# Kernel tuning notes

Measured on AMD Instinct MI355X. Metric: run time of the kernel, lower is better.

## Reference

```python
import jax, jax.numpy as jnp
import numpy as np

B, N, DIN, DH, DOUT, H = 2, 512, 32, 64, 64, 4
NEG_SLOPE = 0.2  # PyG GATv2Conv default
EPS = 1e-5       # LayerNorm eps


def layernorm(y, g, b):
    mu = jnp.mean(y, axis=-1, keepdims=True)
    var = jnp.mean(jnp.square(y - mu), axis=-1, keepdims=True)
    return (y - mu) * jax.lax.rsqrt(var + EPS) * g + b


def gatv2(x, wl, bl, wr, br, att, bias, mask):
    """Dense GATv2 over all-pairs edges given boolean mask [N,N] (j->i)."""
    Bb, Nn, _ = x.shape
    Hh, Dd = att.shape
    xl = (x @ wl + bl).reshape(Bb, Nn, Hh, Dd)  # source features W_l x_j
    xr = (x @ wr + br).reshape(Bb, Nn, Hh, Dd)  # target features W_r x_i
    # e[b,h,i,j] = att_h . leaky_relu(xl[b,j,h] + xr[b,i,h])
    z = jax.nn.leaky_relu(xl[:, None, :, :, :] + xr[:, :, None, :, :], NEG_SLOPE)  # [B,i,j,H,D]
    e = jnp.einsum('bijhd,hd->bhij', z, att)
    e = jnp.where(mask[None, None], e, -jnp.inf)
    alpha = jax.nn.softmax(e, axis=-1)            # softmax over source j per target i
    out = jnp.einsum('bhij,bjhd->bihd', alpha, xl).reshape(Bb, Nn, Hh * Dd)
    return out + bias


def setup_inputs() -> dict:
    key = jax.random.key(0)
    ks = jax.random.split(key, 10)
    s = lambda k, shape: (jax.random.normal(k, shape, dtype=jnp.float32) * 0.1)
    return {
        'x': jax.random.normal(ks[0], (B, N, DIN), dtype=jnp.float32),
        'embedding': jax.random.normal(ks[1], (N, DH), dtype=jnp.float32),
        # gat1: in_dim -> hidden_dim, 4 heads, concat
        'w1_l': s(ks[2], (DIN, H * DH)), 'b1_l': jnp.zeros((H * DH,), jnp.float32),
        'w1_r': s(ks[3], (DIN, H * DH)), 'b1_r': jnp.zeros((H * DH,), jnp.float32),
        'att1': s(ks[4], (H, DH)), 'bias1': jnp.zeros((H * DH,), jnp.float32),
        'g1': jnp.ones((H * DH,), jnp.float32), 'be1': jnp.zeros((H * DH,), jnp.float32),
        # gat2: 4*hidden_dim -> out_dim, 4 heads, concat
        'w2_l': s(ks[5], (H * DH, H * DOUT)), 'b2_l': jnp.zeros((H * DOUT,), jnp.float32),
        'w2_r': s(ks[6], (H * DH, H * DOUT)), 'b2_r': jnp.zeros((H * DOUT,), jnp.float32),
        'att2': s(ks[7], (H, DOUT)), 'bias2': jnp.zeros((H * DOUT,), jnp.float32),
        'g2': jnp.ones((H * DOUT,), jnp.float32), 'be2': jnp.zeros((H * DOUT,), jnp.float32),
    }


def reference(x, embedding, w1_l, b1_l, w1_r, b1_r, att1, bias1, g1, be1,
              w2_l, b2_l, w2_r, b2_r, att2, bias2, g2, be2):
    # AdaptiveAdjacency: cosine-similarity adjacency; only its nonzero
    # PATTERN is used (edge_index = adj.nonzero()); self-loops added by GATv2Conv.
    ne = embedding * jax.lax.rsqrt(jnp.sum(embedding * embedding, axis=1, keepdims=True))
    adj = ne @ ne.T
    mask = (adj != 0) | jnp.eye(N, dtype=bool)
    h = gatv2(x, w1_l, b1_l, w1_r, b1_r, att1, bias1, mask)
    h = jax.nn.relu(layernorm(h, g1, be1))
    # dropout(p=0.3) is identity in eval mode
    out = gatv2(h, w2_l, b2_l, w2_r, b2_r, att2, bias2, mask)
    out = layernorm(out, g2, be2)
    return out
```

## Files before the change

kernel.cpp:

```cpp
#include <hip/hip_runtime.h>


#define BB   2
#define NN   512
#define DIN  32
#define DH   64
#define HH   4
#define C1   256
#define C2   256
#define NJC  4
#define LEPS 1e-5f

typedef unsigned long long u64;

__device__ __forceinline__ float bf_sum(float v) {
#pragma unroll
    for (int o = 32; o > 0; o >>= 1) v += __shfl_xor(v, o, 64);
    return v;
}

__device__ __forceinline__ void gload_lds16(const float* g, float* l) {
    __builtin_amdgcn_global_load_lds(
        (const __attribute__((address_space(1))) void*)g,
        (__attribute__((address_space(3))) void*)l, 16, 0, 0);
}

__device__ __forceinline__ float rdlane(float v, int l) {
    return __int_as_float(__builtin_amdgcn_readlane(__float_as_int(v), l));
}

__global__ __launch_bounds__(256) void mask_k(const float* __restrict__ emb,
                                              u64* __restrict__ mask64) {
    __shared__ __align__(16) float s_ei[16][DH];
    __shared__ float ebuf[64][DH + 1];
    int it = blockIdx.x, jq = blockIdx.y;
    int t = threadIdx.x, lane = t & 63, iq = t >> 6;
    int j0 = jq * 64;
    {
        int row = t >> 4, d4 = (t & 15) << 2;
        *(float4*)&s_ei[row][d4] = *(const float4*)(emb + (it * 16 + row) * DH + d4);
    }
#pragma unroll
    for (int k = 0; k < 4; k++) {
        int idx = k * 256 + t, jl = idx >> 4, d4 = (idx & 15) << 2;
        float4 v = *(const float4*)(emb + (j0 + jl) * DH + d4);
        ebuf[jl][d4] = v.x; ebuf[jl][d4 + 1] = v.y;
        ebuf[jl][d4 + 2] = v.z; ebuf[jl][d4 + 3] = v.w;
    }
    __syncthreads();
    float acc[4] = {0.f, 0.f, 0.f, 0.f};
    for (int dc = 0; dc < 16; dc++) {
        int d = dc * 4;
        float e0 = ebuf[lane][d], e1 = ebuf[lane][d + 1];
        float e2 = ebuf[lane][d + 2], e3 = ebuf[lane][d + 3];
#pragma unroll
        for (int r = 0; r < 4; r++) {
            float4 iv = *(const float4*)&s_ei[iq * 4 + r][d];
            acc[r] += iv.x * e0 + iv.y * e1 + iv.z * e2 + iv.w * e3;
        }
    }
    int jg = j0 + lane;
#pragma unroll
    for (int r = 0; r < 4; r++) {
        int ig = it * 16 + iq * 4 + r;
        u64 bal = __ballot(acc[r] != 0.f || ig == jg);
        if (lane == 0) mask64[ig * 8 + jq] = bal;
    }
}

__global__ __launch_bounds__(256) void proj1_k(const float* __restrict__ x,
        const float* __restrict__ wl, const float* __restrict__ bl,
        const float* __restrict__ wr, const float* __restrict__ br,
        const float* __restrict__ att,
        float* __restrict__ xl, float* __restrict__ xr,
        float* __restrict__ sl, float* __restrict__ sr) {
    __shared__ float s_x[4][DIN];
    int t = threadIdx.x, lane = t & 63, row0 = blockIdx.x * 4, cq = blockIdx.y;
    if (t < 128) s_x[t >> 5][t & 31] = x[(row0 + (t >> 5)) * DIN + (t & 31)];
    __syncthreads();
    int cl = t & 127, half = t >> 7;
    int gc = cq * 128 + cl;
    const float* wbase; float bias; float* obase; float* sdst; int oc;
    if (gc < C1) { wbase = wl + gc; bias = bl[gc]; obase = xl; sdst = sl; oc = gc; }
    else         { wbase = wr + gc - C1; bias = br[gc - C1]; obase = xr; sdst = sr; oc = gc - C1; }
    int ra = half * 2, rb = ra + 1;
    float a0 = bias, a1 = bias;
#pragma unroll
    for (int k = 0; k < DIN; k++) {
        float wv = wbase[(size_t)k * C1];
        a0 += s_x[ra][k] * wv;
        a1 += s_x[rb][k] * wv;
    }
    obase[(size_t)(row0 + ra) * C1 + oc] = a0;
    obase[(size_t)(row0 + rb) * C1 + oc] = a1;
    float attv = att[oc];
    float s0 = bf_sum(attv * a0) * 0.6f;
    float s1 = bf_sum(attv * a1) * 0.6f;
    if (lane == 0) {
        int h = oc >> 6;
        int rwa = row0 + ra, rwb = row0 + rb;
        sdst[(h * BB + (rwa >> 9)) * NN + (rwa & 511)] = s0;
        sdst[(h * BB + (rwb >> 9)) * NN + (rwb & 511)] = s1;
    }
}

__global__ __launch_bounds__(256) void projln_k(const float* __restrict__ pagg,
        const float* __restrict__ plsum, const float* __restrict__ abias,
        const float* __restrict__ g, const float* __restrict__ be,
        const float* __restrict__ wl, const float* __restrict__ bl,
        const float* __restrict__ wr, const float* __restrict__ br,
        const float* __restrict__ att,
        float* __restrict__ xl, float* __restrict__ xr,
        float* __restrict__ sl, float* __restrict__ sr) {
    __shared__ __align__(16) float s_h[4][C1];
    int t = threadIdx.x, lane = t & 63, w = t >> 6;
    int row0 = blockIdx.x * 4, cq = blockIdx.y;
    {
        int rgb = row0 + w;
        int bb = rgb >> 9, ii = rgb & 511;
        int c4 = lane << 2, hh = lane >> 4;
        float vx = 0.f, vy = 0.f, vz = 0.f, vw = 0.f, l = 0.f;
#pragma unroll
        for (int jc = 0; jc < NJC; jc++) {
            float4 a = *(const float4*)(pagg + ((size_t)jc * BB * NN + rgb) * C1 + c4);
            vx += a.x; vy += a.y; vz += a.z; vw += a.w;
            l += plsum[((size_t)jc * HH * BB + hh * BB + bb) * NN + ii];
        }
        float inv = 1.f / l;
        float4 bi = *(const float4*)(abias + c4);
        vx = vx * inv + bi.x; vy = vy * inv + bi.y;
        vz = vz * inv + bi.z; vw = vw * inv + bi.w;
        float mu = bf_sum(vx + vy + vz + vw) * (1.f / 256.f);
        float dx = vx - mu, dy = vy - mu, dz = vz - mu, dw = vw - mu;
        float var = bf_sum(dx * dx + dy * dy + dz * dz + dw * dw) * (1.f / 256.f);
        float rs = rsqrtf(var + LEPS);
        float4 gv = *(const float4*)(g + c4);
        float4 bv = *(const float4*)(be + c4);
        float4 y;
        y.x = fmaxf(dx * rs * gv.x + bv.x, 0.f);
        y.y = fmaxf(dy * rs * gv.y + bv.y, 0.f);
        y.z = fmaxf(dz * rs * gv.z + bv.z, 0.f);
        y.w = fmaxf(dw * rs * gv.w + bv.w, 0.f);
        *(float4*)&s_h[w][c4] = y;
    }
    __syncthreads();
    int cl = t & 127, half = t >> 7;
    int gc = cq * 128 + cl;
    const float* wbase; float bias; float* obase; float* sdst; int oc;
    if (gc < C2) { wbase = wl + gc; bias = bl[gc]; obase = xl; sdst = sl; oc = gc; }
    else         { wbase = wr + gc - C2; bias = br[gc - C2]; obase = xr; sdst = sr; oc = gc - C2; }
    int ra = half * 2, rb = ra + 1;
    float a0 = bias, a1 = bias;
#pragma unroll 8
    for (int k = 0; k < C1; k++) {
        float wv = wbase[(size_t)k * C2];
        a0 += s_h[ra][k] * wv;
        a1 += s_h[rb][k] * wv;
    }
    obase[(size_t)(row0 + ra) * C2 + oc] = a0;
    obase[(size_t)(row0 + rb) * C2 + oc] = a1;
    float attv = att[oc];
    float s0 = bf_sum(attv * a0) * 0.6f;
    float s1 = bf_sum(attv * a1) * 0.6f;
    if (lane == 0) {
        int h = oc >> 6;
        int rwa = row0 + ra, rwb = row0 + rb;
        sdst[(h * BB + (rwa >> 9)) * NN + (rwa & 511)] = s0;
        sdst[(h * BB + (rwb >> 9)) * NN + (rwb & 511)] = s1;
    }
}

__global__ __launch_bounds__(256) void attn_k(const float* __restrict__ xl,
        const float* __restrict__ xr, const float* __restrict__ att,
        const u64* __restrict__ mask64,
        const float* __restrict__ sl, const float* __restrict__ sr,
        float* __restrict__ pagg, float* __restrict__ plsum) {
    __shared__ __align__(16) float xbuf[128 * 64];

    int bx = blockIdx.x;
    int it = bx >> 2, jc = bx & 3;
    int h = blockIdx.y, b = blockIdx.z;
    int t = threadIdx.x, lane = t & 63;
    int wu = __builtin_amdgcn_readfirstlane(t >> 6);
    int i0 = it * 16, j0 = jc * 128;

    const float* xlbase = xl + (size_t)b * NN * C1 + h * DH;

    {
        int jr0 = wu * 32;
#pragma unroll
        for (int k = 0; k < 8; k++) {
            int jrow = jr0 + k * 4 + (lane >> 4);
            int dslot = (lane & 15) ^ (jrow & 7);
            const float* gp = xlbase + (size_t)(j0 + jrow) * C1 + (dslot << 2);
            gload_lds16(gp, &xbuf[(jr0 + k * 4) * 64]);
        }
    }

    const float* xrb  = xr + (size_t)(b * NN + i0 + wu * 4) * C1 + h * DH;
    const float* attb = att + h * DH;
    float rsr[4];
#pragma unroll
    for (int r = 0; r < 4; r++) rsr[r] = sr[(h * BB + b) * NN + i0 + wu * 4 + r];

    __syncthreads();

    int swz = lane & 7;
    int c = lane >> 2, e = lane & 3;
    float out[4]  = {0.f, 0.f, 0.f, 0.f};
    float lsum[4] = {0.f, 0.f, 0.f, 0.f};

    for (int ph = 0; ph < 2; ph++) {
        float acc[4] = {0.f, 0.f, 0.f, 0.f};
        const float* xrow = &xbuf[(ph * 64 + lane) * 64];
#pragma unroll 2
        for (int dc = 0; dc < 16; dc++) {
            float4 xv = *(const float4*)(xrow + ((dc ^ swz) << 2));
            float4 av = *(const float4*)(attb + (dc << 2));
#pragma unroll
            for (int r = 0; r < 4; r++) {
                float4 rv = *(const float4*)(xrb + r * C1 + (dc << 2));
                acc[r] = fmaf(av.x, fabsf(xv.x + rv.x), acc[r]);
                acc[r] = fmaf(av.y, fabsf(xv.y + rv.y), acc[r]);
                acc[r] = fmaf(av.z, fabsf(xv.z + rv.z), acc[r]);
                acc[r] = fmaf(av.w, fabsf(xv.w + rv.w), acc[r]);
            }
        }
        float slv = sl[(h * BB + b) * NN + j0 + ph * 64 + lane];
        u64 m0 = mask64[(size_t)(i0 + wu * 4 + 0) * 8 + jc * 2 + ph];
        u64 m1 = mask64[(size_t)(i0 + wu * 4 + 1) * 8 + jc * 2 + ph];
        u64 m2 = mask64[(size_t)(i0 + wu * 4 + 2) * 8 + jc * 2 + ph];
        u64 m3 = mask64[(size_t)(i0 + wu * 4 + 3) * 8 + jc * 2 + ph];
        float p0 = ((m0 >> lane) & 1ull) ? __expf(fmaf(0.4f, acc[0], slv + rsr[0])) : 0.f;
        float p1 = ((m1 >> lane) & 1ull) ? __expf(fmaf(0.4f, acc[1], slv + rsr[1])) : 0.f;
        float p2 = ((m2 >> lane) & 1ull) ? __expf(fmaf(0.4f, acc[2], slv + rsr[2])) : 0.f;
        float p3 = ((m3 >> lane) & 1ull) ? __expf(fmaf(0.4f, acc[3], slv + rsr[3])) : 0.f;
        lsum[0] += p0; lsum[1] += p1; lsum[2] += p2; lsum[3] += p3;

#pragma unroll
        for (int j4 = 0; j4 < 16; j4++) {
            int jb = ph * 64 + j4 * 4;
            float x0 = xbuf[(jb + 0) * 64 + (((c ^ ((jb + 0) & 7)) << 2) | e)];
            float x1 = xbuf[(jb + 1) * 64 + (((c ^ ((jb + 1) & 7)) << 2) | e)];
            float x2 = xbuf[(jb + 2) * 64 + (((c ^ ((jb + 2) & 7)) << 2) | e)];
            float x3 = xbuf[(jb + 3) * 64 + (((c ^ ((jb + 3) & 7)) << 2) | e)];
            out[0] += rdlane(p0, j4 * 4 + 0) * x0 + rdlane(p0, j4 * 4 + 1) * x1
                    + rdlane(p0, j4 * 4 + 2) * x2 + rdlane(p0, j4 * 4 + 3) * x3;
            out[1] += rdlane(p1, j4 * 4 + 0) * x0 + rdlane(p1, j4 * 4 + 1) * x1
                    + rdlane(p1, j4 * 4 + 2) * x2 + rdlane(p1, j4 * 4 + 3) * x3;
            out[2] += rdlane(p2, j4 * 4 + 0) * x0 + rdlane(p2, j4 * 4 + 1) * x1
                    + rdlane(p2, j4 * 4 + 2) * x2 + rdlane(p2, j4 * 4 + 3) * x3;
            out[3] += rdlane(p3, j4 * 4 + 0) * x0 + rdlane(p3, j4 * 4 + 1) * x1
                    + rdlane(p3, j4 * 4 + 2) * x2 + rdlane(p3, j4 * 4 + 3) * x3;
        }
    }

    size_t ob = ((size_t)jc * BB * NN + b * NN + i0 + wu * 4) * C1 + h * DH + lane;
#pragma unroll
    for (int r = 0; r < 4; r++) {
        float l = bf_sum(lsum[r]);
        pagg[ob + (size_t)r * C1] = out[r];
        if (lane == 0)
            plsum[((size_t)jc * HH * BB + h * BB + b) * NN + i0 + wu * 4 + r] = l;
    }
}

__global__ __launch_bounds__(256) void ln2_k(const float* __restrict__ pagg,
        const float* __restrict__ plsum, const float* __restrict__ abias,
        const float* __restrict__ g, const float* __restrict__ be,
        float* __restrict__ outp) {
    int t = threadIdx.x, lane = t & 63, w = t >> 6;
    int rgb = blockIdx.x * 4 + w;
    int bb = rgb >> 9, ii = rgb & 511;
    int c4 = lane << 2, hh = lane >> 4;
    float vx = 0.f, vy = 0.f, vz = 0.f, vw = 0.f, l = 0.f;
#pragma unroll
    for (int jc = 0; jc < NJC; jc++) {
        float4 a = *(const float4*)(pagg + ((size_t)jc * BB * NN + rgb) * C1 + c4);
        vx += a.x; vy += a.y; vz += a.z; vw += a.w;
        l += plsum[((size_t)jc * HH * BB + hh * BB + bb) * NN + ii];
    }
    float inv = 1.f / l;
    float4 bi = *(const float4*)(abias + c4);
    vx = vx * inv + bi.x; vy = vy * inv + bi.y;
    vz = vz * inv + bi.z; vw = vw * inv + bi.w;
    float mu = bf_sum(vx + vy + vz + vw) * (1.f / 256.f);
    float dx = vx - mu, dy = vy - mu, dz = vz - mu, dw = vw - mu;
    float var = bf_sum(dx * dx + dy * dy + dz * dz + dw * dw) * (1.f / 256.f);
    float rs = rsqrtf(var + LEPS);
    float4 gv = *(const float4*)(g + c4);
    float4 bv = *(const float4*)(be + c4);
    float4 y;
    y.x = dx * rs * gv.x + bv.x;
    y.y = dy * rs * gv.y + bv.y;
    y.z = dz * rs * gv.z + bv.z;
    y.w = dw * rs * gv.w + bv.w;
    *(float4*)(outp + (size_t)rgb * C1 + c4) = y;
}

extern "C" void kernel_launch(void* const* d_in, const int* in_sizes, int n_in,
                              void* d_out, int out_size, void* d_ws, size_t ws_size,
                              hipStream_t stream) {
    const float* x    = (const float*)d_in[0];
    const float* emb  = (const float*)d_in[1];
    const float* w1l  = (const float*)d_in[2];
    const float* b1l  = (const float*)d_in[3];
    const float* w1r  = (const float*)d_in[4];
    const float* b1r  = (const float*)d_in[5];
    const float* att1 = (const float*)d_in[6];
    const float* bia1 = (const float*)d_in[7];
    const float* g1   = (const float*)d_in[8];
    const float* be1  = (const float*)d_in[9];
    const float* w2l  = (const float*)d_in[10];
    const float* b2l  = (const float*)d_in[11];
    const float* w2r  = (const float*)d_in[12];
    const float* b2r  = (const float*)d_in[13];
    const float* att2 = (const float*)d_in[14];
    const float* bia2 = (const float*)d_in[15];
    const float* g2   = (const float*)d_in[16];
    const float* be2  = (const float*)d_in[17];

    char* w = (char*)d_ws;
    float* xl    = (float*)w; w += (size_t)BB * NN * C1 * 4;
    float* xr    = (float*)w; w += (size_t)BB * NN * C1 * 4;
    float* pagg  = (float*)w; w += (size_t)NJC * BB * NN * C1 * 4;
    u64* mask64  = (u64*)w;   w += (size_t)NN * 8 * 8;
    float* plsum = (float*)w; w += (size_t)NJC * HH * BB * NN * 4;
    float* sl    = (float*)w; w += (size_t)HH * BB * NN * 4;
    float* sr    = (float*)w; w += (size_t)HH * BB * NN * 4;

    mask_k<<<dim3(NN / 16, 8), 256, 0, stream>>>(emb, mask64);
    proj1_k<<<dim3(BB * NN / 4, 4), 256, 0, stream>>>(x, w1l, b1l, w1r, b1r, att1, xl, xr, sl, sr);
    attn_k<<<dim3((NN / 16) * NJC, HH, BB), 256, 0, stream>>>(xl, xr, att1, mask64, sl, sr, pagg, plsum);
    projln_k<<<dim3(BB * NN / 4, 4), 256, 0, stream>>>(pagg, plsum, bia1, g1, be1,
                                                       w2l, b2l, w2r, b2r, att2, xl, xr, sl, sr);
    attn_k<<<dim3((NN / 16) * NJC, HH, BB), 256, 0, stream>>>(xl, xr, att2, mask64, sl, sr, pagg, plsum);
    ln2_k<<<BB * NN / 4, 256, 0, stream>>>(pagg, plsum, bia2, g2, be2, (float*)d_out);
}
```

Baseline: 159.4 us.

## Fuse mask and layer-1 projection kernels; stage xr/att in LDS and restructure attention loops

Merges the adjacency-mask kernel and the first projection kernel into a single launch by splitting the grid on block index, which saves one kernel launch. In the attention kernel, the target-row features and the pre-scaled attention vector are staged in shared memory instead of being re-read from global memory. Mask words, sl and sr values are now loaded up front. Both 64-column halves are computed in one pass with eight accumulators, and the aggregation loop is regrouped to batch 16 LDS reads at a time. This raises register pressure and adds a branch between the two roles inside the fused kernel.

```diff
diff --git a/kernel.cpp b/kernel.cpp
--- a/kernel.cpp
+++ b/kernel.cpp
@@ -29,53 +29,56 @@
     return __int_as_float(__builtin_amdgcn_readlane(__float_as_int(v), l));
 }
 
-__global__ __launch_bounds__(256) void mask_k(const float* __restrict__ emb,
-                                              u64* __restrict__ mask64) {
+__global__ __launch_bounds__(256) void mp1_k(const float* __restrict__ x,
+        const float* __restrict__ wl, const float* __restrict__ bl,
+        const float* __restrict__ wr, const float* __restrict__ br,
+        const float* __restrict__ att, const float* __restrict__ emb,
+        float* __restrict__ xl, float* __restrict__ xr,
+        float* __restrict__ sl, float* __restrict__ sr,
+        u64* __restrict__ mask64) {
     __shared__ __align__(16) float s_ei[16][DH];
     __shared__ float ebuf[64][DH + 1];
-    int it = blockIdx.x, jq = blockIdx.y;
-    int t = threadIdx.x, lane = t & 63, iq = t >> 6;
-    int j0 = jq * 64;
-    {
-        int row = t >> 4, d4 = (t & 15) << 2;
-        *(float4*)&s_ei[row][d4] = *(const float4*)(emb + (it * 16 + row) * DH + d4);
-    }
-#pragma unroll
-    for (int k = 0; k < 4; k++) {
-        int idx = k * 256 + t, jl = idx >> 4, d4 = (idx & 15) << 2;
-        float4 v = *(const float4*)(emb + (j0 + jl) * DH + d4);
-        ebuf[jl][d4] = v.x; ebuf[jl][d4 + 1] = v.y;
-        ebuf[jl][d4 + 2] = v.z; ebuf[jl][d4 + 3] = v.w;
-    }
-    __syncthreads();
-    float acc[4] = {0.f, 0.f, 0.f, 0.f};
-    for (int dc = 0; dc < 16; dc++) {
-        int d = dc * 4;
-        float e0 = ebuf[lane][d], e1 = ebuf[lane][d + 1];
-        float e2 = ebuf[lane][d + 2], e3 = ebuf[lane][d + 3];
+    __shared__ float s_x[4][DIN];
+    int bx = blockIdx.x;
+    int t = threadIdx.x, lane = t & 63;
+
+    if (bx >= 1024) {
+        int idx = bx - 1024, it = idx >> 3, jq = idx & 7;
+        int iq = t >> 6, j0 = jq * 64;
+        {
+            int row = t >> 4, d4 = (t & 15) << 2;
+            *(float4*)&s_ei[row][d4] = *(const float4*)(emb + (it * 16 + row) * DH + d4);
+        }
+#pragma unroll
+        for (int k = 0; k < 4; k++) {
+            int i2 = k * 256 + t, jl = i2 >> 4, d4 = (i2 & 15) << 2;
+            float4 v = *(const float4*)(emb + (j0 + jl) * DH + d4);
+            ebuf[jl][d4] = v.x; ebuf[jl][d4 + 1] = v.y;
+            ebuf[jl][d4 + 2] = v.z; ebuf[jl][d4 + 3] = v.w;
+        }
+        __syncthreads();
+        float acc[4] = {0.f, 0.f, 0.f, 0.f};
+        for (int dc = 0; dc < 16; dc++) {
+            int d = dc * 4;
+            float e0 = ebuf[lane][d], e1 = ebuf[lane][d + 1];
+            float e2 = ebuf[lane][d + 2], e3 = ebuf[lane][d + 3];
+#pragma unroll
+            for (int r = 0; r < 4; r++) {
+                float4 iv = *(const float4*)&s_ei[iq * 4 + r][d];
+                acc[r] += iv.x * e0 + iv.y * e1 + iv.z * e2 + iv.w * e3;
+            }
+        }
+        int jg = j0 + lane;
 #pragma unroll
         for (int r = 0; r < 4; r++) {
-            float4 iv = *(const float4*)&s_ei[iq * 4 + r][d];
-            acc[r] += iv.x * e0 + iv.y * e1 + iv.z * e2 + iv.w * e3;
-        }
-    }
-    int jg = j0 + lane;
-#pragma unroll
-    for (int r = 0; r < 4; r++) {
-        int ig = it * 16 + iq * 4 + r;
-        u64 bal = __ballot(acc[r] != 0.f || ig == jg);
-        if (lane == 0) mask64[ig * 8 + jq] = bal;
-    }
-}
-
-__global__ __launch_bounds__(256) void proj1_k(const float* __restrict__ x,
-        const float* __restrict__ wl, const float* __restrict__ bl,
-        const float* __restrict__ wr, const float* __restrict__ br,
-        const float* __restrict__ att,
-        float* __restrict__ xl, float* __restrict__ xr,
-        float* __restrict__ sl, float* __restrict__ sr) {
-    __shared__ float s_x[4][DIN];
-    int t = threadIdx.x, lane = t & 63, row0 = blockIdx.x * 4, cq = blockIdx.y;
+            int ig = it * 16 + iq * 4 + r;
+            u64 bal = __ballot(acc[r] != 0.f || ig == jg);
+            if (lane == 0) mask64[ig * 8 + jq] = bal;
+        }
+        return;
+    }
+
+    int row0 = (bx >> 2) * 4, cq = bx & 3;
     if (t < 128) s_x[t >> 5][t & 31] = x[(row0 + (t >> 5)) * DIN + (t & 31)];
     __syncthreads();
     int cl = t & 127, half = t >> 7;
@@ -176,6 +179,8 @@
         const float* __restrict__ sl, const float* __restrict__ sr,
         float* __restrict__ pagg, float* __restrict__ plsum) {
     __shared__ __align__(16) float xbuf[128 * 64];
+    __shared__ __align__(16) float s_xr[16][DH];
+    __shared__ __align__(16) float s_att[DH];
 
     int bx = blockIdx.x;
     int it = bx >> 2, jc = bx & 3;
@@ -196,72 +201,108 @@
             gload_lds16(gp, &xbuf[(jr0 + k * 4) * 64]);
         }
     }
-
-    const float* xrb  = xr + (size_t)(b * NN + i0 + wu * 4) * C1 + h * DH;
-    const float* attb = att + h * DH;
-    float rsr[4];
-#pragma unroll
-    for (int r = 0; r < 4; r++) rsr[r] = sr[(h * BB + b) * NN + i0 + wu * 4 + r];
+    {
+        int row = t >> 4, d4 = (t & 15) << 2;
+        *(float4*)&s_xr[row][d4] =
+            *(const float4*)(xr + (size_t)(b * NN + i0 + row) * C1 + h * DH + d4);
+    }
+    if (t < DH) s_att[t] = att[h * DH + t] * 0.4f;
+
+    int rbase = (h * BB + b) * NN;
+    float rsr0 = sr[rbase + i0 + wu * 4 + 0];
+    float rsr1 = sr[rbase + i0 + wu * 4 + 1];
+    float rsr2 = sr[rbase + i0 + wu * 4 + 2];
+    float rsr3 = sr[rbase + i0 + wu * 4 + 3];
+    const u64* mb_ = mask64 + (size_t)(i0 + wu * 4) * 8 + jc * 2;
+    u64 m00 = mb_[0],  m01 = mb_[1];
+    u64 m10 = mb_[8],  m11 = mb_[9];
+    u64 m20 = mb_[16], m21 = mb_[17];
+    u64 m30 = mb_[24], m31 = mb_[25];
+    unsigned mb0 = (unsigned)((m00 >> lane) & 1ull) | ((unsigned)((m01 >> lane) & 1ull) << 1);
+    unsigned mb1 = (unsigned)((m10 >> lane) & 1ull) | ((unsigned)((m11 >> lane) & 1ull) << 1);
+    unsigned mb2 = (unsigned)((m20 >> lane) & 1ull) | ((unsigned)((m21 >> lane) & 1ull) << 1);
+    unsigned mb3 = (unsigned)((m30 >> lane) & 1ull) | ((unsigned)((m31 >> lane) & 1ull) << 1);
+    float slv0 = sl[rbase + j0 + lane];
+    float slv1 = sl[rbase + j0 + 64 + lane];
 
     __syncthreads();
 
     int swz = lane & 7;
-    int c = lane >> 2, e = lane & 3;
-    float out[4]  = {0.f, 0.f, 0.f, 0.f};
-    float lsum[4] = {0.f, 0.f, 0.f, 0.f};
-
-    for (int ph = 0; ph < 2; ph++) {
-        float acc[4] = {0.f, 0.f, 0.f, 0.f};
-        const float* xrow = &xbuf[(ph * 64 + lane) * 64];
-#pragma unroll 2
-        for (int dc = 0; dc < 16; dc++) {
-            float4 xv = *(const float4*)(xrow + ((dc ^ swz) << 2));
-            float4 av = *(const float4*)(attb + (dc << 2));
-#pragma unroll
-            for (int r = 0; r < 4; r++) {
-                float4 rv = *(const float4*)(xrb + r * C1 + (dc << 2));
-                acc[r] = fmaf(av.x, fabsf(xv.x + rv.x), acc[r]);
-                acc[r] = fmaf(av.y, fabsf(xv.y + rv.y), acc[r]);
-                acc[r] = fmaf(av.z, fabsf(xv.z + rv.z), acc[r]);
-                acc[r] = fmaf(av.w, fabsf(xv.w + rv.w), acc[r]);
-            }
-        }
-        float slv = sl[(h * BB + b) * NN + j0 + ph * 64 + lane];
-        u64 m0 = mask64[(size_t)(i0 + wu * 4 + 0) * 8 + jc * 2 + ph];
-        u64 m1 = mask64[(size_t)(i0 + wu * 4 + 1) * 8 + jc * 2 + ph];
-        u64 m2 = mask64[(size_t)(i0 + wu * 4 + 2) * 8 + jc * 2 + ph];
-        u64 m3 = mask64[(size_t)(i0 + wu * 4 + 3) * 8 + jc * 2 + ph];
-        float p0 = ((m0 >> lane) & 1ull) ? __expf(fmaf(0.4f, acc[0], slv + rsr[0])) : 0.f;
-        float p1 = ((m1 >> lane) & 1ull) ? __expf(fmaf(0.4f, acc[1], slv + rsr[1])) : 0.f;
-        float p2 = ((m2 >> lane) & 1ull) ? __expf(fmaf(0.4f, acc[2], slv + rsr[2])) : 0.f;
-        float p3 = ((m3 >> lane) & 1ull) ? __expf(fmaf(0.4f, acc[3], slv + rsr[3])) : 0.f;
-        lsum[0] += p0; lsum[1] += p1; lsum[2] += p2; lsum[3] += p3;
-
-#pragma unroll
-        for (int j4 = 0; j4 < 16; j4++) {
-            int jb = ph * 64 + j4 * 4;
-            float x0 = xbuf[(jb + 0) * 64 + (((c ^ ((jb + 0) & 7)) << 2) | e)];
-            float x1 = xbuf[(jb + 1) * 64 + (((c ^ ((jb + 1) & 7)) << 2) | e)];
-            float x2 = xbuf[(jb + 2) * 64 + (((c ^ ((jb + 2) & 7)) << 2) | e)];
-            float x3 = xbuf[(jb + 3) * 64 + (((c ^ ((jb + 3) & 7)) << 2) | e)];
-            out[0] += rdlane(p0, j4 * 4 + 0) * x0 + rdlane(p0, j4 * 4 + 1) * x1
-                    + rdlane(p0, j4 * 4 + 2) * x2 + rdlane(p0, j4 * 4 + 3) * x3;
-            out[1] += rdlane(p1, j4 * 4 + 0) * x0 + rdlane(p1, j4 * 4 + 1) * x1
-                    + rdlane(p1, j4 * 4 + 2) * x2 + rdlane(p1, j4 * 4 + 3) * x3;
-            out[2] += rdlane(p2, j4 * 4 + 0) * x0 + rdlane(p2, j4 * 4 + 1) * x1
-                    + rdlane(p2, j4 * 4 + 2) * x2 + rdlane(p2, j4 * 4 + 3) * x3;
-            out[3] += rdlane(p3, j4 * 4 + 0) * x0 + rdlane(p3, j4 * 4 + 1) * x1
-                    + rdlane(p3, j4 * 4 + 2) * x2 + rdlane(p3, j4 * 4 + 3) * x3;
-        }
-    }
-
+    int cc = lane >> 2, e = lane & 3;
+
+    float a00=0,a01=0,a02=0,a03=0;
+    float a10=0,a11=0,a12=0,a13=0;
+    const float* xr0 = &xbuf[lane * 64];
+    const float* xr1 = &xbuf[(64 + lane) * 64];
+#pragma unroll 4
+    for (int dc = 0; dc < 16; dc++) {
+        int so = (dc ^ swz) << 2;
+        float4 xv0 = *(const float4*)(xr0 + so);
+        float4 xv1 = *(const float4*)(xr1 + so);
+        float4 av  = *(const float4*)&s_att[dc << 2];
+        float4 r0  = *(const float4*)&s_xr[wu * 4 + 0][dc << 2];
+        float4 r1  = *(const float4*)&s_xr[wu * 4 + 1][dc << 2];
+        float4 r2  = *(const float4*)&s_xr[wu * 4 + 2][dc << 2];
+        float4 r3  = *(const float4*)&s_xr[wu * 4 + 3][dc << 2];
+        a00 = fmaf(av.x, fabsf(xv0.x + r0.x), a00); a00 = fmaf(av.y, fabsf(xv0.y + r0.y), a00);
+        a00 = fmaf(av.z, fabsf(xv0.z + r0.z), a00); a00 = fmaf(av.w, fabsf(xv0.w + r0.w), a00);
+        a01 = fmaf(av.x, fabsf(xv0.x + r1.x), a01); a01 = fmaf(av.y, fabsf(xv0.y + r1.y), a01);
+        a01 = fmaf(av.z, fabsf(xv0.z + r1.z), a01); a01 = fmaf(av.w, fabsf(xv0.w + r1.w), a01);
+        a02 = fmaf(av.x, fabsf(xv0.x + r2.x), a02); a02 = fmaf(av.y, fabsf(xv0.y + r2.y), a02);
+        a02 = fmaf(av.z, fabsf(xv0.z + r2.z), a02); a02 = fmaf(av.w, fabsf(xv0.w + r2.w), a02);
+        a03 = fmaf(av.x, fabsf(xv0.x + r3.x), a03); a03 = fmaf(av.y, fabsf(xv0.y + r3.y), a03);
+        a03 = fmaf(av.z, fabsf(xv0.z + r3.z), a03); a03 = fmaf(av.w, fabsf(xv0.w + r3.w), a03);
+        a10 = fmaf(av.x, fabsf(xv1.x + r0.x), a10); a10 = fmaf(av.y, fabsf(xv1.y + r0.y), a10);
+        a10 = fmaf(av.z, fabsf(xv1.z + r0.z), a10); a10 = fmaf(av.w, fabsf(xv1.w + r0.w), a10);
+        a11 = fmaf(av.x, fabsf(xv1.x + r1.x), a11); a11 = fmaf(av.y, fabsf(xv1.y + r1.y), a11);
+        a11 = fmaf(av.z, fabsf(xv1.z + r1.z), a11); a11 = fmaf(av.w, fabsf(xv1.w + r1.w), a11);
+        a12 = fmaf(av.x, fabsf(xv1.x + r2.x), a12); a12 = fmaf(av.y, fabsf(xv1.y + r2.y), a12);
+        a12 = fmaf(av.z, fabsf(xv1.z + r2.z), a12); a12 = fmaf(av.w, fabsf(xv1.w + r2.w), a12);
+        a13 = fmaf(av.x, fabsf(xv1.x + r3.x), a13); a13 = fmaf(av.y, fabsf(xv1.y + r3.y), a13);
+        a13 = fmaf(av.z, fabsf(xv1.z + r3.z), a13); a13 = fmaf(av.w, fabsf(xv1.w + r3.w), a13);
+    }
+
+    float p00 = (mb0 & 1u) ? __expf(slv0 + rsr0 + a00) : 0.f;
+    float p01 = (mb1 & 1u) ? __expf(slv0 + rsr1 + a01) : 0.f;
+    float p02 = (mb2 & 1u) ? __expf(slv0 + rsr2 + a02) : 0.f;
+    float p03 = (mb3 & 1u) ? __expf(slv0 + rsr3 + a03) : 0.f;
+    float p10 = (mb0 & 2u) ? __expf(slv1 + rsr0 + a10) : 0.f;
+    float p11 = (mb1 & 2u) ? __expf(slv1 + rsr1 + a11) : 0.f;
+    float p12 = (mb2 & 2u) ? __expf(slv1 + rsr2 + a12) : 0.f;
+    float p13 = (mb3 & 2u) ? __expf(slv1 + rsr3 + a13) : 0.f;
+    float ls0 = p00 + p10, ls1 = p01 + p11, ls2 = p02 + p12, ls3 = p03 + p13;
+
+    float out0 = 0.f, out1 = 0.f, out2 = 0.f, out3 = 0.f;
+#pragma unroll
+    for (int g = 0; g < 8; g++) {
+        float xb[16];
+#pragma unroll
+        for (int u = 0; u < 16; u++) {
+            int row = g * 16 + u;
+            xb[u] = xbuf[row * 64 + (((cc ^ (u & 7)) << 2) | e)];
+        }
+#pragma unroll
+        for (int u = 0; u < 16; u++) {
+            int li = (g & 3) * 16 + u;
+            float q0, q1, q2, q3;
+            if (g < 4) { q0 = rdlane(p00, li); q1 = rdlane(p01, li);
+                         q2 = rdlane(p02, li); q3 = rdlane(p03, li); }
+            else       { q0 = rdlane(p10, li); q1 = rdlane(p11, li);
+                         q2 = rdlane(p12, li); q3 = rdlane(p13, li); }
+            out0 += q0 * xb[u]; out1 += q1 * xb[u];
+            out2 += q2 * xb[u]; out3 += q3 * xb[u];
+        }
+    }
+
+    float l0 = bf_sum(ls0), l1 = bf_sum(ls1), l2 = bf_sum(ls2), l3 = bf_sum(ls3);
     size_t ob = ((size_t)jc * BB * NN + b * NN + i0 + wu * 4) * C1 + h * DH + lane;
-#pragma unroll
-    for (int r = 0; r < 4; r++) {
-        float l = bf_sum(lsum[r]);
-        pagg[ob + (size_t)r * C1] = out[r];
-        if (lane == 0)
-            plsum[((size_t)jc * HH * BB + h * BB + b) * NN + i0 + wu * 4 + r] = l;
+    pagg[ob]          = out0;
+    pagg[ob + C1]     = out1;
+    pagg[ob + 2 * C1] = out2;
+    pagg[ob + 3 * C1] = out3;
+    if (lane == 0) {
+        float* pl = plsum + ((size_t)jc * HH * BB + h * BB + b) * NN + i0 + wu * 4;
+        pl[0] = l0; pl[1] = l1; pl[2] = l2; pl[3] = l3;
     }
 }
 
@@ -329,8 +370,8 @@
     float* sl    = (float*)w; w += (size_t)HH * BB * NN * 4;
     float* sr    = (float*)w; w += (size_t)HH * BB * NN * 4;
 
-    mask_k<<<dim3(NN / 16, 8), 256, 0, stream>>>(emb, mask64);
-    proj1_k<<<dim3(BB * NN / 4, 4), 256, 0, stream>>>(x, w1l, b1l, w1r, b1r, att1, xl, xr, sl, sr);
+    mp1_k<<<dim3(1280), 256, 0, stream>>>(x, w1l, b1l, w1r, b1r, att1, emb,
+                                          xl, xr, sl, sr, mask64);
     attn_k<<<dim3((NN / 16) * NJC, HH, BB), 256, 0, stream>>>(xl, xr, att1, mask64, sl, sr, pagg, plsum);
     projln_k<<<dim3(BB * NN / 4, 4), 256, 0, stream>>>(pagg, plsum, bia1, g1, be1,
                                                        w2l, b2l, w2r, b2r, att2, xl, xr, sl, sr);
```

After: 160.6 us. About the same (+0.8%).
